# Optimization experiments

Hardware: AMD Instinct MI355X
Metric: run time of the kernel (lower is better)

The kernel has to match this reference:

```python
import jax, jax.numpy as jnp
import numpy as np

D_MODEL = 2048
N_HEADS = 16
HEAD_DIM = D_MODEL // N_HEADS
D_FF = 8192
B, T = 2, 2048
LN_EPS = 1e-5


def layer_norm(x, g, b):
    mu = jnp.mean(x, axis=-1, keepdims=True)
    var = jnp.mean(jnp.square(x - mu), axis=-1, keepdims=True)
    return (x - mu) * jax.lax.rsqrt(var + LN_EPS) * g + b


def setup_inputs() -> dict:
    key = jax.random.key(0)
    ks = jax.random.split(key, 8)
    s = 0.02
    return {
        "x": jax.random.normal(ks[0], (B, T, D_MODEL), dtype=jnp.float32),
        "ln1_g": jnp.ones((D_MODEL,), jnp.float32),
        "ln1_b": jnp.zeros((D_MODEL,), jnp.float32),
        "ln2_g": jnp.ones((D_MODEL,), jnp.float32),
        "ln2_b": jnp.zeros((D_MODEL,), jnp.float32),
        "w_qkv": jax.random.normal(ks[1], (3 * D_MODEL, D_MODEL), jnp.float32) * s,
        "w_out": jax.random.normal(ks[2], (D_MODEL, D_MODEL), jnp.float32) * s,
        "w_up": jax.random.normal(ks[3], (D_FF, D_MODEL), jnp.float32) * s,
        "b_up": jnp.zeros((D_FF,), jnp.float32),
        "w_down": jax.random.normal(ks[4], (D_MODEL, D_FF), jnp.float32) * s,
        "b_down": jnp.zeros((D_MODEL,), jnp.float32),
    }


def reference(x, ln1_g, ln1_b, ln2_g, ln2_b, w_qkv, w_out, w_up, b_up, w_down, b_down):
    b, t, c = x.shape
    # --- attention (pre-norm) ---
    h = layer_norm(x, ln1_g, ln1_b)
    qkv = h @ w_qkv.T                                  # [B,T,3C]
    q, k, v = jnp.split(qkv, 3, axis=-1)
    # [B,H,T,Dh]
    q = q.reshape(b, t, N_HEADS, HEAD_DIM).transpose(0, 2, 1, 3)
    k = k.reshape(b, t, N_HEADS, HEAD_DIM).transpose(0, 2, 1, 3)
    v = v.reshape(b, t, N_HEADS, HEAD_DIM).transpose(0, 2, 1, 3)
    scale = 1.0 / np.sqrt(HEAD_DIM).astype(np.float32)
    attn = jnp.einsum("bhqd,bhkd->bhqk", q, k) * scale
    causal = jnp.tril(jnp.ones((t, t), dtype=bool))
    attn = jnp.where(causal, attn, jnp.float32(-jnp.inf))
    attn = jax.nn.softmax(attn, axis=-1)
    out = jnp.einsum("bhqk,bhkd->bhqd", attn, v)
    out = out.transpose(0, 2, 1, 3).reshape(b, t, c)
    x = x + out @ w_out.T
    # --- FFN (pre-norm, GeLU exact) ---
    h = layer_norm(x, ln2_g, ln2_b)
    h = jax.nn.gelu(h @ w_up.T + b_up, approximate=False)
    x = x + h @ w_down.T + b_down
    return x
```

## Files before the change

kernel.cpp:

```cpp
#include <hip/hip_runtime.h>
#include <cstdint>
#include <cstddef>

using u16 = unsigned short;
typedef __attribute__((ext_vector_type(8))) __bf16 bf16x8;
typedef __attribute__((ext_vector_type(4))) float f32x4;

__device__ inline u16 f2bf(float f) {
  union { float f; unsigned u; } v; v.f = f;
  unsigned r = (v.u + 0x7fffu + ((v.u >> 16) & 1u)) >> 16;
  return (u16)r;
}

__device__ inline float bf2f(u16 u) {
  union { unsigned u; float f; } v; v.u = (unsigned)u << 16;
  return v.f;
}

#define GLDS(g, s) __builtin_amdgcn_global_load_lds( \
    (__attribute__((address_space(1))) void*)(g), \
    (__attribute__((address_space(3))) void*)(s), 16, 0, 0)

__global__ __launch_bounds__(256) void cvt_bf16(const float* __restrict__ in,
                                                u16* __restrict__ out, int n8) {
  int i = blockIdx.x * 256 + threadIdx.x;
  if (i >= n8) return;
  float4 v0 = *(const float4*)&in[(size_t)i * 8];
  float4 v1 = *(const float4*)&in[(size_t)i * 8 + 4];
  union { u16 u[8]; uint4 q; } pk;
  pk.u[0] = f2bf(v0.x); pk.u[1] = f2bf(v0.y); pk.u[2] = f2bf(v0.z); pk.u[3] = f2bf(v0.w);
  pk.u[4] = f2bf(v1.x); pk.u[5] = f2bf(v1.y); pk.u[6] = f2bf(v1.z); pk.u[7] = f2bf(v1.w);
  *(uint4*)&out[(size_t)i * 8] = pk.q;
}

__global__ __launch_bounds__(256) void ln_bf16(const float* __restrict__ x,
                                               const float* __restrict__ g,
                                               const float* __restrict__ bsh,
                                               u16* __restrict__ out) {
  __shared__ float red[8];
  int tid = threadIdx.x;
  int lane = tid & 63, w = tid >> 6;
  size_t row = blockIdx.x;
  const float* xr = x + row * 2048;
  float4 v0 = *(const float4*)&xr[tid * 8];
  float4 v1 = *(const float4*)&xr[tid * 8 + 4];
  float s = v0.x + v0.y + v0.z + v0.w + v1.x + v1.y + v1.z + v1.w;
  float s2 = v0.x*v0.x + v0.y*v0.y + v0.z*v0.z + v0.w*v0.w
           + v1.x*v1.x + v1.y*v1.y + v1.z*v1.z + v1.w*v1.w;
#pragma unroll
  for (int m = 1; m < 64; m <<= 1) { s += __shfl_xor(s, m); s2 += __shfl_xor(s2, m); }
  if (lane == 0) { red[w] = s; red[w + 4] = s2; }
  __syncthreads();
  s = red[0] + red[1] + red[2] + red[3];
  s2 = red[4] + red[5] + red[6] + red[7];
  float mu = s * (1.0f / 2048.0f);
  float var = s2 * (1.0f / 2048.0f) - mu * mu;
  float rs = rsqrtf(var + 1e-5f);
  float4 g0 = *(const float4*)&g[tid * 8];
  float4 g1 = *(const float4*)&g[tid * 8 + 4];
  float4 b0 = *(const float4*)&bsh[tid * 8];
  float4 b1 = *(const float4*)&bsh[tid * 8 + 4];
  float xv[8] = {v0.x, v0.y, v0.z, v0.w, v1.x, v1.y, v1.z, v1.w};
  float gv[8] = {g0.x, g0.y, g0.z, g0.w, g1.x, g1.y, g1.z, g1.w};
  float bv[8] = {b0.x, b0.y, b0.z, b0.w, b1.x, b1.y, b1.z, b1.w};
  union { u16 u[8]; uint4 q; } pk;
#pragma unroll
  for (int j = 0; j < 8; j++) pk.u[j] = f2bf((xv[j] - mu) * rs * gv[j] + bv[j]);
  *(uint4*)&out[row * 2048 + tid * 8] = pk.q;
}

__global__ __launch_bounds__(256) void combine4h(const u16* __restrict__ p,
                                                 const float* __restrict__ resid,
                                                 const float* __restrict__ bias,
                                                 float* __restrict__ out, int n8) {
  int stride = gridDim.x * 256;
  for (int i = blockIdx.x * 256 + threadIdx.x; i < n8; i += stride) {
    size_t base = (size_t)i * 8;
    float s[8];
    float4 r0 = *(const float4*)&resid[base];
    float4 r1 = *(const float4*)&resid[base + 4];
    s[0]=r0.x; s[1]=r0.y; s[2]=r0.z; s[3]=r0.w;
    s[4]=r1.x; s[5]=r1.y; s[6]=r1.z; s[7]=r1.w;
    if (bias) {
      int col0 = (int)(base & 2047);
      float4 b0 = *(const float4*)&bias[col0];
      float4 b1 = *(const float4*)&bias[col0 + 4];
      s[0]+=b0.x; s[1]+=b0.y; s[2]+=b0.z; s[3]+=b0.w;
      s[4]+=b1.x; s[5]+=b1.y; s[6]+=b1.z; s[7]+=b1.w;
    }
#pragma unroll
    for (int k = 0; k < 4; ++k) {
      union { uint4 q; u16 u[8]; } v;
      v.q = *(const uint4*)&p[(size_t)k * 8388608 + base];
#pragma unroll
      for (int j = 0; j < 8; ++j) s[j] += bf2f(v.u[j]);
    }
    float4 o0 = {s[0], s[1], s[2], s[3]};
    float4 o1 = {s[4], s[5], s[6], s[7]};
    *(float4*)&out[base] = o0;
    *(float4*)&out[base + 4] = o1;
  }
}

template <int EPI, int LDK, int KLEN, int NSPLIT>
__global__ __launch_bounds__(512, 4) void gemm_bk32(
    const u16* __restrict__ A, const u16* __restrict__ B,
    int M, int N, const float* __restrict__ bias, u16* __restrict__ outh,
    int xc, int chr, int chc) {
  __shared__ u16 lds[36864];
  constexpr int NT = KLEN / 32;
  int tid = threadIdx.x;
  int lane = tid & 63, wid = tid >> 6;
  int wr = wid >> 2, wc = wid & 3;
  int lr = lane & 15, lg = lane >> 4;

  int sub = blockIdx.x;
  if (NSPLIT > 1) {
    int per = (M >> 7) * (N >> 8);
    int ks = sub / per;
    sub -= ks * per;
    A += (size_t)ks * KLEN;
    B += (size_t)ks * KLEN;
    outh += (size_t)ks * M * N;
  }
  int xcd = sub & 7, slot = sub >> 3;
  int rr = slot / chc, cc = slot - rr * chc;
  int by = (xcd / xc) * chr + rr;
  int bx = (xcd - (xcd / xc) * xc) * chc + cc;
  size_t bm = (size_t)by * 128, bn = (size_t)bx * 256;

  const u16* Ablk = A + bm * LDK;
  const u16* Bblk = B + bn * LDK;

  int sA = (tid >> 2) * LDK + (((tid & 3) ^ ((tid >> 3) & 3)) * 8);
  int gs = (lg ^ ((lr >> 1) & 3)) * 8;
  int aoff = (wr * 64 + lr) * 32 + gs;
  int boff = 4096 + (wc * 64 + lr) * 32 + gs;

  f32x4 acc[4][4];
#pragma unroll
  for (int mq = 0; mq < 4; ++mq)
#pragma unroll
    for (int nq = 0; nq < 4; ++nq) acc[mq][nq] = (f32x4){0.f, 0.f, 0.f, 0.f};

  bf16x8 af[4], bfr[4];

#define STAGE(bb, tt) do { \
    const u16* As = Ablk + (tt) * 32 + sA; \
    const u16* Bs = Bblk + (tt) * 32 + sA; \
    GLDS(As, &lds[(bb) * 12288 + tid * 8]); \
    GLDS(Bs, &lds[(bb) * 12288 + 4096 + tid * 8]); \
    GLDS(Bs + 128 * (size_t)LDK, &lds[(bb) * 12288 + 8192 + tid * 8]); \
  } while (0)
#define BARS do { __builtin_amdgcn_s_barrier(); __builtin_amdgcn_sched_barrier(0); } while (0)

  STAGE(0, 0);
  STAGE(1, 1);

  int c = 0;
  for (int t = 0; t < NT; ++t) {
    if (t + 1 < NT) {
      asm volatile("s_waitcnt vmcnt(3)" ::: "memory");
    } else {
      asm volatile("s_waitcnt vmcnt(0)" ::: "memory");
    }
    BARS;
#pragma unroll
    for (int mq = 0; mq < 4; ++mq)
      af[mq] = *(const bf16x8*)&lds[c * 12288 + mq * 512 + aoff];
#pragma unroll
    for (int nq = 0; nq < 4; ++nq)
      bfr[nq] = *(const bf16x8*)&lds[c * 12288 + nq * 512 + boff];
    if (t + 2 < NT) {
      int cs = c + 2; if (cs >= 3) cs -= 3;
      STAGE(cs, t + 2);
    }
    __builtin_amdgcn_s_setprio(1);
#pragma unroll
    for (int mq = 0; mq < 4; ++mq)
#pragma unroll
      for (int nq = 0; nq < 4; ++nq)
        acc[mq][nq] = __builtin_amdgcn_mfma_f32_16x16x32_bf16(af[mq], bfr[nq], acc[mq][nq], 0, 0, 0);
    __builtin_amdgcn_s_setprio(0);
    c = (c == 2) ? 0 : c + 1;
  }

#undef STAGE
#undef BARS

  size_t row0 = bm + wr * 64, col0 = bn + wc * 64;
#pragma unroll
  for (int mq = 0; mq < 4; ++mq) {
#pragma unroll
    for (int nq = 0; nq < 4; ++nq) {
#pragma unroll
      for (int r = 0; r < 4; ++r) {
        size_t row = row0 + mq * 16 + lg * 4 + r;
        size_t col = col0 + nq * 16 + lr;
        size_t idx = row * (size_t)N + col;
        float v = acc[mq][nq][r];
        if (EPI == 0) {
          outh[idx] = f2bf(v);
        } else {
          v += bias[col];
          outh[idx] = f2bf(0.5f * v * (1.0f + erff(v * 0.70710678118654752f)));
        }
      }
    }
  }
}

__global__ __launch_bounds__(256) void vtrans(const u16* __restrict__ qkv,
                                              u16* __restrict__ vt) {
  __shared__ u16 tile[32][33];
  int tx = threadIdx.x & 31, ty = threadIdx.x >> 5;
  int t0 = blockIdx.x * 32, d0 = blockIdx.y * 32, bh = blockIdx.z;
  int b = bh >> 4, h = bh & 15;
  const u16* src = qkv + (size_t)b * 2048 * 6144 + 4096 + h * 128 + d0;
#pragma unroll
  for (int i = 0; i < 4; i++)
    tile[ty + i * 8][tx] = src[(size_t)(t0 + ty + i * 8) * 6144 + tx];
  __syncthreads();
  u16* dst = vt + (size_t)bh * 128 * 2048 + (size_t)d0 * 2048 + t0;
#pragma unroll
  for (int i = 0; i < 4; i++)
    dst[(size_t)(ty + i * 8) * 2048 + tx] = tile[tx][ty + i * 8];
}

__device__ inline void stage_kv(const u16* __restrict__ ktok, const u16* __restrict__ vbase,
                                int k0, u16* kb, u16* vb, int tid) {
#pragma unroll
  for (int c = 0; c < 4; ++c) {
    int s = c * 256 + tid;
    int r = s >> 4, g = s & 15;
    const u16* src = ktok + (size_t)(k0 + r) * 6144 + ((g ^ (r & 7)) * 8);
    GLDS(src, &kb[s * 8]);
  }
#pragma unroll
  for (int c = 0; c < 4; ++c) {
    int s = c * 256 + tid;
    int d = s >> 3, g = s & 7;
    const u16* src = vbase + (size_t)d * 2048 + k0 + ((g ^ (d & 7)) * 8);
    GLDS(src, &vb[s * 8]);
  }
}

__global__ __launch_bounds__(256) void attn_fwd(const u16* __restrict__ qkv,
                                                const u16* __restrict__ vt,
                                                u16* __restrict__ outh) {
  __shared__ u16 kbuf[2][8192];
  __shared__ u16 vbuf[2][8192];
  __shared__ u16 p_lds[4][1024];
  int tid = threadIdx.x, lane = tid & 63, w = tid >> 6;
  int lr = lane & 15, lg = lane >> 4;
  int bh = blockIdx.x, p = blockIdx.y;
  int b = bh >> 4, h = bh & 15;
  const float scale = 0.08838834764831845f;
  const u16* tokbase = qkv + (size_t)b * 2048 * 6144;
  const u16* ktok = tokbase + 2048 + h * 128;
  const u16* vbase = vt + (size_t)bh * 262144;
  u16* pl = p_lds[w];

  for (int half = 0; half < 2; ++half) {
    int qt = (half == 0) ? p : 31 - p;
    int qbase = qt * 64 + w * 16;
    int nt = qt + 1;

    bf16x8 qf[4];
    const u16* qrow_ptr = tokbase + (size_t)(qbase + lr) * 6144 + h * 128;
#pragma unroll
    for (int kk = 0; kk < 4; kk++) qf[kk] = *(const bf16x8*)&qrow_ptr[kk * 32 + lg * 8];

    f32x4 o[8];
#pragma unroll
    for (int d = 0; d < 8; d++) o[d] = (f32x4){0.f, 0.f, 0.f, 0.f};
    float mrow[4] = {-1e30f, -1e30f, -1e30f, -1e30f};
    float lsum[4] = {0.f, 0.f, 0.f, 0.f};

    int cur = 0;
    stage_kv(ktok, vbase, 0, kbuf[0], vbuf[0], tid);
    __syncthreads();

    for (int t = 0; t < nt; ++t) {
      int k0 = t * 64;
      if (t + 1 < nt) stage_kv(ktok, vbase, k0 + 64, kbuf[cur ^ 1], vbuf[cur ^ 1], tid);
      const u16* kb = kbuf[cur];
      const u16* vb = vbuf[cur];

      f32x4 s[4];
#pragma unroll
      for (int c = 0; c < 4; c++) s[c] = (f32x4){0.f, 0.f, 0.f, 0.f};
#pragma unroll
      for (int kk = 0; kk < 4; kk++) {
#pragma unroll
        for (int c = 0; c < 4; c++) {
          bf16x8 kf = *(const bf16x8*)&kb[(c * 16 + lr) * 128 + (((kk * 4 + lg) ^ (lr & 7)) * 8)];
          s[c] = __builtin_amdgcn_mfma_f32_16x16x32_bf16(qf[kk], kf, s[c], 0, 0, 0);
        }
      }

      float mt[4];
#pragma unroll
      for (int r = 0; r < 4; r++) {
        int qrow = qbase + lg * 4 + r;
        float m = -1e30f;
#pragma unroll
        for (int c = 0; c < 4; c++) {
          int key = k0 + c * 16 + lr;
          float v = (key <= qrow) ? s[c][r] * scale : -1e30f;
          s[c][r] = v;
          m = fmaxf(m, v);
        }
        mt[r] = m;
      }
#pragma unroll
      for (int msk = 1; msk < 16; msk <<= 1)
#pragma unroll
        for (int r = 0; r < 4; r++) mt[r] = fmaxf(mt[r], __shfl_xor(mt[r], msk));
      float al[4], ps[4];
#pragma unroll
      for (int r = 0; r < 4; r++) {
        float mn = fmaxf(mrow[r], mt[r]);
        al[r] = __expf(mrow[r] - mn);
        mrow[r] = mn;
        float sum = 0.f;
#pragma unroll
        for (int c = 0; c < 4; c++) {
          float pv = __expf(s[c][r] - mn);
          s[c][r] = pv;
          sum += pv;
        }
        ps[r] = sum;
      }
#pragma unroll
      for (int msk = 1; msk < 16; msk <<= 1)
#pragma unroll
        for (int r = 0; r < 4; r++) ps[r] += __shfl_xor(ps[r], msk);
#pragma unroll
      for (int r = 0; r < 4; r++) lsum[r] = lsum[r] * al[r] + ps[r];
#pragma unroll
      for (int d = 0; d < 8; d++)
#pragma unroll
        for (int r = 0; r < 4; r++) o[d][r] *= al[r];

#pragma unroll
      for (int r = 0; r < 4; r++) {
        int prow = lg * 4 + r;
#pragma unroll
        for (int c = 0; c < 4; c++) {
          int gw = (c * 2 + (lr >> 3)) ^ (prow & 7);
          pl[prow * 64 + gw * 8 + (lr & 7)] = f2bf(s[c][r]);
        }
      }
      asm volatile("s_waitcnt lgkmcnt(0)" ::: "memory");
      bf16x8 pa[2];
#pragma unroll
      for (int ks = 0; ks < 2; ks++)
        pa[ks] = *(const bf16x8*)&pl[lr * 64 + (((ks * 4 + lg) ^ (lr & 7)) * 8)];
#pragma unroll
      for (int dt = 0; dt < 8; dt++) {
#pragma unroll
        for (int ks = 0; ks < 2; ks++) {
          bf16x8 vf = *(const bf16x8*)&vb[(dt * 16 + lr) * 64 + (((ks * 4 + lg) ^ (lr & 7)) * 8)];
          o[dt] = __builtin_amdgcn_mfma_f32_16x16x32_bf16(pa[ks], vf, o[dt], 0, 0, 0);
        }
      }
      __syncthreads();
      cur ^= 1;
    }

    float inv[4];
#pragma unroll
    for (int r = 0; r < 4; r++) inv[r] = 1.0f / lsum[r];
    u16* ob = outh + (size_t)(b * 2048 + qbase) * 2048 + h * 128;
#pragma unroll
    for (int dt = 0; dt < 8; dt++)
#pragma unroll
      for (int r = 0; r < 4; r++)
        ob[(size_t)(lg * 4 + r) * 2048 + dt * 16 + lr] = f2bf(o[dt][r] * inv[r]);
  }
}

extern "C" void kernel_launch(void* const* d_in, const int* in_sizes, int n_in,
                              void* d_out, int out_size, void* d_ws, size_t ws_size,
                              hipStream_t stream) {
  const float* x      = (const float*)d_in[0];
  const float* ln1_g  = (const float*)d_in[1];
  const float* ln1_b  = (const float*)d_in[2];
  const float* ln2_g  = (const float*)d_in[3];
  const float* ln2_b  = (const float*)d_in[4];
  const float* w_qkv  = (const float*)d_in[5];
  const float* w_out  = (const float*)d_in[6];
  const float* w_up   = (const float*)d_in[7];
  const float* b_up   = (const float*)d_in[8];
  const float* w_down = (const float*)d_in[9];
  const float* b_down = (const float*)d_in[10];
  float* outp = (float*)d_out;

  char* ws = (char*)d_ws;
  u16* w_qkv_bf  = (u16*)(ws + 0);
  u16* w_out_bf  = (u16*)(ws + 25165824);
  u16* w_up_bf   = (u16*)(ws + 33554432);
  u16* w_down_bf = (u16*)(ws + 67108864);
  u16* hb        = (u16*)(ws + 100663296);
  u16* qkvb      = (u16*)(ws + 117440512);
  u16* vtb       = (u16*)(ws + 167772160);
  u16* ub        = (u16*)(ws + 117440512);
  float* x1      = (float*)(ws + 184549376);
  u16* oPartH    = (u16*)(ws + 117440512);
  u16* dPartH    = (u16*)(ws + 0);

  cvt_bf16<<<6144, 256, 0, stream>>>(w_qkv, w_qkv_bf, 1572864);
  cvt_bf16<<<2048, 256, 0, stream>>>(w_out, w_out_bf, 524288);
  cvt_bf16<<<8192, 256, 0, stream>>>(w_up, w_up_bf, 2097152);
  cvt_bf16<<<8192, 256, 0, stream>>>(w_down, w_down_bf, 2097152);

  ln_bf16<<<4096, 256, 0, stream>>>(x, ln1_g, ln1_b, hb);
  gemm_bk32<0, 2048, 2048, 1><<<768, 512, 0, stream>>>(hb, w_qkv_bf, 4096, 6144,
                                                       nullptr, qkvb, 4, 16, 6);
  vtrans<<<dim3(64, 4, 32), 256, 0, stream>>>(qkvb, vtb);
  attn_fwd<<<dim3(32, 16), 256, 0, stream>>>(qkvb, vtb, hb);
  gemm_bk32<0, 2048, 512, 4><<<1024, 512, 0, stream>>>(hb, w_out_bf, 4096, 2048,
                                                       nullptr, oPartH, 2, 8, 4);
  combine4h<<<2048, 256, 0, stream>>>(oPartH, x, nullptr, x1, 1048576);

  ln_bf16<<<4096, 256, 0, stream>>>(x1, ln2_g, ln2_b, hb);
  gemm_bk32<2, 2048, 2048, 1><<<1024, 512, 0, stream>>>(hb, w_up_bf, 4096, 8192,
                                                        b_up, ub, 4, 16, 8);
  gemm_bk32<0, 8192, 2048, 4><<<1024, 512, 0, stream>>>(ub, w_down_bf, 4096, 2048,
                                                        nullptr, dPartH, 2, 8, 4);
  combine4h<<<2048, 256, 0, stream>>>(dPartH, x1, b_down, outp, 1048576);
}
```

Measured before the change: 645.2 us.

## Use 256x256 GEMM tiles, halve split-K, and write fp32 partials

The GEMM block tile grows from 128x256 to 256x256, with 8x4 MFMA accumulators per wave and a larger LDS buffer. The goal is to raise arithmetic intensity and cut redundant global loads. Split-K for the out-projection and down-projection drops from 4 to 2, and partials are now stored as fp32 rather than bf16, with a simpler two-input combine kernel. In exchange, register pressure is higher, the min-occupancy launch bound is gone, the grids are smaller (256 blocks for the split GEMMs, which may underfill the 256 CUs), and partial traffic in fp32 is larger per element.

```diff
diff --git a/kernel.cpp b/kernel.cpp
--- a/kernel.cpp
+++ b/kernel.cpp
@@ -10,11 +10,6 @@
   union { float f; unsigned u; } v; v.f = f;
   unsigned r = (v.u + 0x7fffu + ((v.u >> 16) & 1u)) >> 16;
   return (u16)r;
-}
-
-__device__ inline float bf2f(u16 u) {
-  union { unsigned u; float f; } v; v.u = (unsigned)u << 16;
-  return v.f;
 }
 
 #define GLDS(g, s) __builtin_amdgcn_global_load_lds( \
@@ -69,45 +64,35 @@
   *(uint4*)&out[row * 2048 + tid * 8] = pk.q;
 }
 
-__global__ __launch_bounds__(256) void combine4h(const u16* __restrict__ p,
-                                                 const float* __restrict__ resid,
-                                                 const float* __restrict__ bias,
-                                                 float* __restrict__ out, int n8) {
+__global__ __launch_bounds__(256) void combine2(const float* __restrict__ a,
+                                                const float* __restrict__ b,
+                                                const float* __restrict__ resid,
+                                                const float* __restrict__ bias,
+                                                float* __restrict__ out, int n4) {
   int stride = gridDim.x * 256;
-  for (int i = blockIdx.x * 256 + threadIdx.x; i < n8; i += stride) {
-    size_t base = (size_t)i * 8;
-    float s[8];
-    float4 r0 = *(const float4*)&resid[base];
-    float4 r1 = *(const float4*)&resid[base + 4];
-    s[0]=r0.x; s[1]=r0.y; s[2]=r0.z; s[3]=r0.w;
-    s[4]=r1.x; s[5]=r1.y; s[6]=r1.z; s[7]=r1.w;
+  for (int i = blockIdx.x * 256 + threadIdx.x; i < n4; i += stride) {
+    float4 va = ((const float4*)a)[i];
+    float4 vb = ((const float4*)b)[i];
+    float4 vr = ((const float4*)resid)[i];
+    float4 o;
+    o.x = va.x + vb.x + vr.x; o.y = va.y + vb.y + vr.y;
+    o.z = va.z + vb.z + vr.z; o.w = va.w + vb.w + vr.w;
     if (bias) {
-      int col0 = (int)(base & 2047);
-      float4 b0 = *(const float4*)&bias[col0];
-      float4 b1 = *(const float4*)&bias[col0 + 4];
-      s[0]+=b0.x; s[1]+=b0.y; s[2]+=b0.z; s[3]+=b0.w;
-      s[4]+=b1.x; s[5]+=b1.y; s[6]+=b1.z; s[7]+=b1.w;
+      int col0 = (i * 4) & 2047;
+      float4 bb = *(const float4*)&bias[col0];
+      o.x += bb.x; o.y += bb.y; o.z += bb.z; o.w += bb.w;
     }
-#pragma unroll
-    for (int k = 0; k < 4; ++k) {
-      union { uint4 q; u16 u[8]; } v;
-      v.q = *(const uint4*)&p[(size_t)k * 8388608 + base];
-#pragma unroll
-      for (int j = 0; j < 8; ++j) s[j] += bf2f(v.u[j]);
-    }
-    float4 o0 = {s[0], s[1], s[2], s[3]};
-    float4 o1 = {s[4], s[5], s[6], s[7]};
-    *(float4*)&out[base] = o0;
-    *(float4*)&out[base + 4] = o1;
+    ((float4*)out)[i] = o;
   }
 }
 
 template <int EPI, int LDK, int KLEN, int NSPLIT>
-__global__ __launch_bounds__(512, 4) void gemm_bk32(
+__global__ __launch_bounds__(512) void gemm256b(
     const u16* __restrict__ A, const u16* __restrict__ B,
-    int M, int N, const float* __restrict__ bias, u16* __restrict__ outh,
+    int M, int N, const float* __restrict__ bias,
+    float* __restrict__ outf, u16* __restrict__ outh,
     int xc, int chr, int chc) {
-  __shared__ u16 lds[36864];
+  __shared__ u16 lds[49152];
   constexpr int NT = KLEN / 32;
   int tid = threadIdx.x;
   int lane = tid & 63, wid = tid >> 6;
@@ -116,41 +101,46 @@
 
   int sub = blockIdx.x;
   if (NSPLIT > 1) {
-    int per = (M >> 7) * (N >> 8);
+    int per = (M >> 8) * (N >> 8);
     int ks = sub / per;
     sub -= ks * per;
     A += (size_t)ks * KLEN;
     B += (size_t)ks * KLEN;
-    outh += (size_t)ks * M * N;
+    outf += (size_t)ks * M * N;
   }
   int xcd = sub & 7, slot = sub >> 3;
   int rr = slot / chc, cc = slot - rr * chc;
   int by = (xcd / xc) * chr + rr;
   int bx = (xcd - (xcd / xc) * xc) * chc + cc;
-  size_t bm = (size_t)by * 128, bn = (size_t)bx * 256;
+  size_t bm = (size_t)by * 256, bn = (size_t)bx * 256;
 
   const u16* Ablk = A + bm * LDK;
   const u16* Bblk = B + bn * LDK;
 
-  int sA = (tid >> 2) * LDK + (((tid & 3) ^ ((tid >> 3) & 3)) * 8);
+  int sOff[2];
+#pragma unroll
+  for (int c = 0; c < 2; ++c) {
+    int s = tid + c * 512;
+    int row = s >> 2, g = s & 3;
+    sOff[c] = row * LDK + ((g ^ ((row >> 1) & 3)) * 8);
+  }
   int gs = (lg ^ ((lr >> 1) & 3)) * 8;
-  int aoff = (wr * 64 + lr) * 32 + gs;
-  int boff = 4096 + (wc * 64 + lr) * 32 + gs;
-
-  f32x4 acc[4][4];
-#pragma unroll
-  for (int mq = 0; mq < 4; ++mq)
+  int aoff = (wr * 128 + lr) * 32 + gs;
+  int boff = 8192 + (wc * 64 + lr) * 32 + gs;
+
+  f32x4 acc[8][4];
+#pragma unroll
+  for (int mq = 0; mq < 8; ++mq)
 #pragma unroll
     for (int nq = 0; nq < 4; ++nq) acc[mq][nq] = (f32x4){0.f, 0.f, 0.f, 0.f};
 
-  bf16x8 af[4], bfr[4];
+  bf16x8 af[8], bfr[4];
 
 #define STAGE(bb, tt) do { \
-    const u16* As = Ablk + (tt) * 32 + sA; \
-    const u16* Bs = Bblk + (tt) * 32 + sA; \
-    GLDS(As, &lds[(bb) * 12288 + tid * 8]); \
-    GLDS(Bs, &lds[(bb) * 12288 + 4096 + tid * 8]); \
-    GLDS(Bs + 128 * (size_t)LDK, &lds[(bb) * 12288 + 8192 + tid * 8]); \
+    GLDS(Ablk + (tt) * 32 + sOff[0], &lds[(bb) * 16384 + tid * 8]); \
+    GLDS(Ablk + (tt) * 32 + sOff[1], &lds[(bb) * 16384 + 4096 + tid * 8]); \
+    GLDS(Bblk + (tt) * 32 + sOff[0], &lds[(bb) * 16384 + 8192 + tid * 8]); \
+    GLDS(Bblk + (tt) * 32 + sOff[1], &lds[(bb) * 16384 + 12288 + tid * 8]); \
   } while (0)
 #define BARS do { __builtin_amdgcn_s_barrier(); __builtin_amdgcn_sched_barrier(0); } while (0)
 
@@ -160,24 +150,24 @@
   int c = 0;
   for (int t = 0; t < NT; ++t) {
     if (t + 1 < NT) {
-      asm volatile("s_waitcnt vmcnt(3)" ::: "memory");
+      asm volatile("s_waitcnt vmcnt(4)" ::: "memory");
     } else {
       asm volatile("s_waitcnt vmcnt(0)" ::: "memory");
     }
     BARS;
 #pragma unroll
-    for (int mq = 0; mq < 4; ++mq)
-      af[mq] = *(const bf16x8*)&lds[c * 12288 + mq * 512 + aoff];
+    for (int mq = 0; mq < 8; ++mq)
+      af[mq] = *(const bf16x8*)&lds[c * 16384 + mq * 512 + aoff];
 #pragma unroll
     for (int nq = 0; nq < 4; ++nq)
-      bfr[nq] = *(const bf16x8*)&lds[c * 12288 + nq * 512 + boff];
+      bfr[nq] = *(const bf16x8*)&lds[c * 16384 + nq * 512 + boff];
     if (t + 2 < NT) {
       int cs = c + 2; if (cs >= 3) cs -= 3;
       STAGE(cs, t + 2);
     }
     __builtin_amdgcn_s_setprio(1);
 #pragma unroll
-    for (int mq = 0; mq < 4; ++mq)
+    for (int mq = 0; mq < 8; ++mq)
 #pragma unroll
       for (int nq = 0; nq < 4; ++nq)
         acc[mq][nq] = __builtin_amdgcn_mfma_f32_16x16x32_bf16(af[mq], bfr[nq], acc[mq][nq], 0, 0, 0);
@@ -188,9 +178,9 @@
 #undef STAGE
 #undef BARS
 
-  size_t row0 = bm + wr * 64, col0 = bn + wc * 64;
-#pragma unroll
-  for (int mq = 0; mq < 4; ++mq) {
+  size_t row0 = bm + wr * 128, col0 = bn + wc * 64;
+#pragma unroll
+  for (int mq = 0; mq < 8; ++mq) {
 #pragma unroll
     for (int nq = 0; nq < 4; ++nq) {
 #pragma unroll
@@ -201,9 +191,11 @@
         float v = acc[mq][nq][r];
         if (EPI == 0) {
           outh[idx] = f2bf(v);
-        } else {
+        } else if (EPI == 2) {
           v += bias[col];
           outh[idx] = f2bf(0.5f * v * (1.0f + erff(v * 0.70710678118654752f)));
+        } else if (EPI == 4) {
+          outf[idx] = v;
         }
       }
     }
@@ -407,8 +399,8 @@
   u16* vtb       = (u16*)(ws + 167772160);
   u16* ub        = (u16*)(ws + 117440512);
   float* x1      = (float*)(ws + 184549376);
-  u16* oPartH    = (u16*)(ws + 117440512);
-  u16* dPartH    = (u16*)(ws + 0);
+  float* oPartF  = (float*)(ws + 117440512);
+  float* dPartF  = (float*)(ws + 0);
 
   cvt_bf16<<<6144, 256, 0, stream>>>(w_qkv, w_qkv_bf, 1572864);
   cvt_bf16<<<2048, 256, 0, stream>>>(w_out, w_out_bf, 524288);
@@ -416,18 +408,18 @@
   cvt_bf16<<<8192, 256, 0, stream>>>(w_down, w_down_bf, 2097152);
 
   ln_bf16<<<4096, 256, 0, stream>>>(x, ln1_g, ln1_b, hb);
-  gemm_bk32<0, 2048, 2048, 1><<<768, 512, 0, stream>>>(hb, w_qkv_bf, 4096, 6144,
-                                                       nullptr, qkvb, 4, 16, 6);
+  gemm256b<0, 2048, 2048, 1><<<384, 512, 0, stream>>>(hb, w_qkv_bf, 4096, 6144,
+                                                      nullptr, nullptr, qkvb, 4, 8, 6);
   vtrans<<<dim3(64, 4, 32), 256, 0, stream>>>(qkvb, vtb);
   attn_fwd<<<dim3(32, 16), 256, 0, stream>>>(qkvb, vtb, hb);
-  gemm_bk32<0, 2048, 512, 4><<<1024, 512, 0, stream>>>(hb, w_out_bf, 4096, 2048,
-                                                       nullptr, oPartH, 2, 8, 4);
-  combine4h<<<2048, 256, 0, stream>>>(oPartH, x, nullptr, x1, 1048576);
+  gemm256b<4, 2048, 1024, 2><<<256, 512, 0, stream>>>(hb, w_out_bf, 4096, 2048,
+                                                      nullptr, oPartF, nullptr, 2, 4, 4);
+  combine2<<<2048, 256, 0, stream>>>(oPartF, oPartF + 8388608, x, nullptr, x1, 2097152);
 
   ln_bf16<<<4096, 256, 0, stream>>>(x1, ln2_g, ln2_b, hb);
-  gemm_bk32<2, 2048, 2048, 1><<<1024, 512, 0, stream>>>(hb, w_up_bf, 4096, 8192,
-                                                        b_up, ub, 4, 16, 8);
-  gemm_bk32<0, 8192, 2048, 4><<<1024, 512, 0, stream>>>(ub, w_down_bf, 4096, 2048,
-                                                        nullptr, dPartH, 2, 8, 4);
-  combine4h<<<2048, 256, 0, stream>>>(dPartH, x1, b_down, outp, 1048576);
-}
+  gemm256b<2, 2048, 2048, 1><<<512, 512, 0, stream>>>(hb, w_up_bf, 4096, 8192,
+                                                      b_up, nullptr, ub, 4, 8, 8);
+  gemm256b<4, 8192, 4096, 2><<<256, 512, 0, stream>>>(ub, w_down_bf, 4096, 2048,
+                                                      nullptr, dPartF, nullptr, 2, 4, 4);
+  combine2<<<2048, 256, 0, stream>>>(dPartF, dPartF + 8388608, x1, b_down, outp, 2097152);
+}
```

New measurement: 709.2 us. +9.9%, slower.

## Split-K the QKV GEMM in two and merge weight conversions into one kernel

Applied to the files above, without the earlier changes.

The four weight conversion launches are merged into one grid-stride kernel, saving launch overhead. The QKV projection now uses split-K of 2 with twice as many blocks, writing bf16 partials that a new combine2h kernel sums in place. This raises occupancy for the 768-block GEMM, at the cost of an extra partial buffer round-trip, a second bf16 rounding step, and one more launch. The partial buffer at offset qkvb+25165824 elements must not overlap the vtb region.

```diff
diff --git a/kernel.cpp b/kernel.cpp
--- a/kernel.cpp
+++ b/kernel.cpp
@@ -21,16 +21,26 @@
     (__attribute__((address_space(1))) void*)(g), \
     (__attribute__((address_space(3))) void*)(s), 16, 0, 0)
 
-__global__ __launch_bounds__(256) void cvt_bf16(const float* __restrict__ in,
-                                                u16* __restrict__ out, int n8) {
-  int i = blockIdx.x * 256 + threadIdx.x;
-  if (i >= n8) return;
-  float4 v0 = *(const float4*)&in[(size_t)i * 8];
-  float4 v1 = *(const float4*)&in[(size_t)i * 8 + 4];
-  union { u16 u[8]; uint4 q; } pk;
-  pk.u[0] = f2bf(v0.x); pk.u[1] = f2bf(v0.y); pk.u[2] = f2bf(v0.z); pk.u[3] = f2bf(v0.w);
-  pk.u[4] = f2bf(v1.x); pk.u[5] = f2bf(v1.y); pk.u[6] = f2bf(v1.z); pk.u[7] = f2bf(v1.w);
-  *(uint4*)&out[(size_t)i * 8] = pk.q;
+__global__ __launch_bounds__(256) void cvt_all(const float* __restrict__ a0,
+                                               const float* __restrict__ a1,
+                                               const float* __restrict__ a2,
+                                               const float* __restrict__ a3,
+                                               u16* __restrict__ o0, u16* __restrict__ o1,
+                                               u16* __restrict__ o2, u16* __restrict__ o3) {
+  int stride = gridDim.x * 256;
+  for (int i = blockIdx.x * 256 + threadIdx.x; i < 6291456; i += stride) {
+    const float* in; u16* out; int j = i;
+    if (j < 1572864) { in = a0; out = o0; }
+    else if ((j -= 1572864) < 524288) { in = a1; out = o1; }
+    else if ((j -= 524288) < 2097152) { in = a2; out = o2; }
+    else { j -= 2097152; in = a3; out = o3; }
+    float4 v0 = *(const float4*)&in[(size_t)j * 8];
+    float4 v1 = *(const float4*)&in[(size_t)j * 8 + 4];
+    union { u16 u[8]; uint4 q; } pk;
+    pk.u[0] = f2bf(v0.x); pk.u[1] = f2bf(v0.y); pk.u[2] = f2bf(v0.z); pk.u[3] = f2bf(v0.w);
+    pk.u[4] = f2bf(v1.x); pk.u[5] = f2bf(v1.y); pk.u[6] = f2bf(v1.z); pk.u[7] = f2bf(v1.w);
+    *(uint4*)&out[(size_t)j * 8] = pk.q;
+  }
 }
 
 __global__ __launch_bounds__(256) void ln_bf16(const float* __restrict__ x,
@@ -67,6 +77,20 @@
 #pragma unroll
   for (int j = 0; j < 8; j++) pk.u[j] = f2bf((xv[j] - mu) * rs * gv[j] + bv[j]);
   *(uint4*)&out[row * 2048 + tid * 8] = pk.q;
+}
+
+__global__ __launch_bounds__(256) void combine2h(const u16* p0, const u16* p1,
+                                                 u16* out, int n8) {
+  int stride = gridDim.x * 256;
+  for (int i = blockIdx.x * 256 + threadIdx.x; i < n8; i += stride) {
+    size_t base = (size_t)i * 8;
+    union { uint4 q; u16 u[8]; } a, b, o;
+    a.q = *(const uint4*)&p0[base];
+    b.q = *(const uint4*)&p1[base];
+#pragma unroll
+    for (int j = 0; j < 8; ++j) o.u[j] = f2bf(bf2f(a.u[j]) + bf2f(b.u[j]));
+    *(uint4*)&out[base] = o.q;
+  }
 }
 
 __global__ __launch_bounds__(256) void combine4h(const u16* __restrict__ p,
@@ -410,14 +434,13 @@
   u16* oPartH    = (u16*)(ws + 117440512);
   u16* dPartH    = (u16*)(ws + 0);
 
-  cvt_bf16<<<6144, 256, 0, stream>>>(w_qkv, w_qkv_bf, 1572864);
-  cvt_bf16<<<2048, 256, 0, stream>>>(w_out, w_out_bf, 524288);
-  cvt_bf16<<<8192, 256, 0, stream>>>(w_up, w_up_bf, 2097152);
-  cvt_bf16<<<8192, 256, 0, stream>>>(w_down, w_down_bf, 2097152);
+  cvt_all<<<4096, 256, 0, stream>>>(w_qkv, w_out, w_up, w_down,
+                                    w_qkv_bf, w_out_bf, w_up_bf, w_down_bf);
 
   ln_bf16<<<4096, 256, 0, stream>>>(x, ln1_g, ln1_b, hb);
-  gemm_bk32<0, 2048, 2048, 1><<<768, 512, 0, stream>>>(hb, w_qkv_bf, 4096, 6144,
-                                                       nullptr, qkvb, 4, 16, 6);
+  gemm_bk32<0, 2048, 1024, 2><<<1536, 512, 0, stream>>>(hb, w_qkv_bf, 4096, 6144,
+                                                        nullptr, qkvb, 4, 16, 6);
+  combine2h<<<2048, 256, 0, stream>>>(qkvb, qkvb + 25165824, qkvb, 3145728);
   vtrans<<<dim3(64, 4, 32), 256, 0, stream>>>(qkvb, vtb);
   attn_fwd<<<dim3(32, 16), 256, 0, stream>>>(qkvb, vtb, hb);
   gemm_bk32<0, 2048, 512, 4><<<1024, 512, 0, stream>>>(hb, w_out_bf, 4096, 2048,
```

Result: slower. 669.4 us (+3.8%).
